# Performance work log

Hardware: AMD Instinct MI355X
Metric: run time of the kernel (lower is better)

## Reference

```python
import math
import jax, jax.numpy as jnp
import numpy as np

H = 1024
NH = 16
HD = H // NH
FF = 4096


def gelu_erf(x):
    return x * 0.5 * (1.0 + jax.lax.erf(x / jnp.sqrt(jnp.float32(2.0))))


def layernorm(x, gamma, beta, eps=1e-12):
    mean = x.mean(axis=-1, keepdims=True)
    var = ((x - mean) ** 2).mean(axis=-1, keepdims=True)
    return gamma * (x - mean) / jnp.sqrt(var + eps) + beta


def setup_inputs() -> dict:
    key = jax.random.key(0)
    ks = jax.random.split(key, 12)
    B, S = 2, 2048
    sc = 0.02
    return {
        "x": jax.random.normal(ks[0], (B, S, H), jnp.float32),
        "attention_mask": jnp.ones((B, S), jnp.int32),
        "Wq": jax.random.normal(ks[1], (H, H), jnp.float32) * sc,
        "bq": jnp.zeros((H,), jnp.float32),
        "Wk": jax.random.normal(ks[2], (H, H), jnp.float32) * sc,
        "bk": jnp.zeros((H,), jnp.float32),
        "Wv": jax.random.normal(ks[3], (H, H), jnp.float32) * sc,
        "bv": jnp.zeros((H,), jnp.float32),
        "Wo": jax.random.normal(ks[4], (H, H), jnp.float32) * sc,
        "bo": jnp.zeros((H,), jnp.float32),
        "ln1_g": jnp.ones((H,), jnp.float32),
        "ln1_b": jnp.zeros((H,), jnp.float32),
        "W1": jax.random.normal(ks[5], (H, FF), jnp.float32) * sc,
        "b1": jnp.zeros((FF,), jnp.float32),
        "W2": jax.random.normal(ks[6], (FF, H), jnp.float32) * sc,
        "b2": jnp.zeros((H,), jnp.float32),
        "ln2_g": jnp.ones((H,), jnp.float32),
        "ln2_b": jnp.zeros((H,), jnp.float32),
    }


def reference(x, attention_mask, Wq, bq, Wk, bk, Wv, bv, Wo, bo,
              ln1_g, ln1_b, W1, b1, W2, b2, ln2_g, ln2_b):
    B, S, _ = x.shape
    # QKV projections, split heads -> [B, NH, S, HD]
    def split(t):
        return t.reshape(B, S, NH, HD).transpose(0, 2, 1, 3)
    q = split(x @ Wq + bq)
    k = split(x @ Wk + bk)
    v = split(x @ Wv + bv)
    # scores [B, NH, S, S]
    s = jnp.einsum("bhqd,bhkd->bhqk", q, k) / math.sqrt(HD)
    mask = (attention_mask == 1)[:, None, None, :]  # [B,1,1,S]
    s = jnp.where(mask, s, -jnp.inf)
    p = jax.nn.softmax(s, axis=-1)
    a = jnp.einsum("bhqk,bhkd->bhqd", p, v)
    a = a.transpose(0, 2, 1, 3).reshape(B, S, H)  # merge heads
    a = a @ Wo + bo
    a = layernorm(a, ln1_g, ln1_b)  # NOTE: no residual in source
    m = gelu_erf(a @ W1 + b1) @ W2 + b2
    return layernorm(m, ln2_g, ln2_b)
```

## Files before the change

kernel.cpp:

```cpp
#include <hip/hip_runtime.h>
#include <hip/hip_bf16.h>
#include <math.h>

typedef __bf16 bf16;
typedef __attribute__((ext_vector_type(8))) __bf16 bf16x8;
typedef __attribute__((ext_vector_type(4))) __bf16 bf16x4;
typedef __attribute__((ext_vector_type(4))) float f32x4;

#define HDIM 1024
#define NHEAD 16
#define HD 64
#define FFDIM 4096
#define BATCH 2
#define SEQ 2048
#define M_TOK 4096
#define PSTRIDE ((size_t)M_TOK * HDIM)

static __device__ __forceinline__ void async_load16(const bf16* g, bf16* l) {
  __builtin_amdgcn_global_load_lds(
      (const __attribute__((address_space(1))) void*)g,
      (__attribute__((address_space(3))) void*)l, 16, 0, 0);
}

__global__ __launch_bounds__(256)
void cast_f32_to_bf16(const float* __restrict__ in, bf16* __restrict__ out)
{
  const size_t i = ((size_t)blockIdx.x * 256 + threadIdx.x) * 4;
  f32x4 v = *(const f32x4*)(in + i);
  bf16x4 o;
#pragma unroll
  for (int j = 0; j < 4; ++j) o[j] = (bf16)v[j];
  *(bf16x4*)(out + i) = o;
}

__global__ __launch_bounds__(256)
void transpose_cast(const float* __restrict__ in, bf16* __restrict__ out, int R, int C)
{
  __shared__ float tile[32][33];
  const int tx = threadIdx.x & 31, ty = threadIdx.x >> 5;
  const int c0 = blockIdx.x * 32, r0 = blockIdx.y * 32;
#pragma unroll
  for (int i = 0; i < 32; i += 8)
    tile[ty + i][tx] = in[(size_t)(r0 + ty + i) * C + c0 + tx];
  __syncthreads();
#pragma unroll
  for (int i = 0; i < 32; i += 8)
    out[(size_t)(c0 + ty + i) * R + r0 + tx] = (bf16)tile[tx][ty + i];
}

__global__ __launch_bounds__(256)
void transpose_cast4(const float* __restrict__ s0, const float* __restrict__ s1,
                     const float* __restrict__ s2, const float* __restrict__ s3,
                     bf16* __restrict__ dstBase)
{
  __shared__ float tile[32][33];
  const int z = blockIdx.z;
  const float* in = (z == 0) ? s0 : (z == 1) ? s1 : (z == 2) ? s2 : s3;
  bf16* out = dstBase + (size_t)z * HDIM * HDIM;
  const int tx = threadIdx.x & 31, ty = threadIdx.x >> 5;
  const int c0 = blockIdx.x * 32, r0 = blockIdx.y * 32;
#pragma unroll
  for (int i = 0; i < 32; i += 8)
    tile[ty + i][tx] = in[(size_t)(r0 + ty + i) * HDIM + c0 + tx];
  __syncthreads();
#pragma unroll
  for (int i = 0; i < 32; i += 8)
    out[(size_t)(c0 + ty + i) * HDIM + r0 + tx] = (bf16)tile[tx][ty + i];
}

template<int EPI>
__global__ __launch_bounds__(256)
void gemm_bt(const bf16* __restrict__ A, const bf16* __restrict__ Bt,
             const float* __restrict__ bias, void* __restrict__ Cout,
             int M, int N, int ldk, int kchunk)
{
  __shared__ __align__(16) bf16 As[128 * 64];
  __shared__ __align__(16) bf16 Bs[128 * 64];
  const int t = threadIdx.x;
  const int wave = t >> 6, lane = t & 63;
  const int lm = lane & 15, qd = lane >> 4;
  const int wm = (wave >> 1) * 64, wn = (wave & 1) * 64;
  const int bm = blockIdx.y * 128, bn = blockIdx.x * 128;
  const int kbeg = blockIdx.z * kchunk;

  f32x4 acc[4][4] = {};
  const int srow = t >> 3;
  const int schk = t & 7;

  for (int k0 = kbeg; k0 < kbeg + kchunk; k0 += 64) {
#pragma unroll
    for (int r = 0; r < 4; ++r) {
      const int row = r * 32 + srow;
      const int chunk = schk ^ (row & 7);
      async_load16(A + (size_t)(bm + row) * ldk + (k0 + chunk * 8),
                   (bf16*)((char*)As + r * 4096 + t * 16));
    }
#pragma unroll
    for (int r = 0; r < 4; ++r) {
      const int row = r * 32 + srow;
      const int chunk = schk ^ (row & 7);
      async_load16(Bt + (size_t)(bn + row) * ldk + (k0 + chunk * 8),
                   (bf16*)((char*)Bs + r * 4096 + t * 16));
    }
    __syncthreads();
#pragma unroll
    for (int ks = 0; ks < 2; ++ks) {
      bf16x8 av[4], bv[4];
#pragma unroll
      for (int mt = 0; mt < 4; ++mt) {
        const int row = wm + mt * 16 + lm;
        const int chunk = (ks * 4 + qd) ^ (row & 7);
        av[mt] = *(const bf16x8*)(As + row * 64 + chunk * 8);
      }
#pragma unroll
      for (int nt = 0; nt < 4; ++nt) {
        const int row = wn + nt * 16 + lm;
        const int chunk = (ks * 4 + qd) ^ (row & 7);
        bv[nt] = *(const bf16x8*)(Bs + row * 64 + chunk * 8);
      }
#pragma unroll
      for (int mt = 0; mt < 4; ++mt)
#pragma unroll
        for (int nt = 0; nt < 4; ++nt)
          acc[mt][nt] = __builtin_amdgcn_mfma_f32_16x16x32_bf16(av[mt], bv[nt], acc[mt][nt], 0, 0, 0);
    }
    __syncthreads();
  }

#pragma unroll
  for (int nt = 0; nt < 4; ++nt) {
    const int col = bn + wn + nt * 16 + lm;
    const float bs = (EPI == 1) ? 0.f : bias[col];
#pragma unroll
    for (int mt = 0; mt < 4; ++mt) {
#pragma unroll
      for (int r = 0; r < 4; ++r) {
        const int row = bm + wm + mt * 16 + qd * 4 + r;
        float v = acc[mt][nt][r] + bs;
        if (EPI == 1) {
          ((float*)Cout + (size_t)blockIdx.z * M * N)[(size_t)row * N + col] = v;
        } else if (EPI == 2) {
          float g = v * 0.5f * (1.0f + erff(v * 0.70710678118f));
          ((bf16*)Cout)[(size_t)row * N + col] = (bf16)g;
        } else {
          bf16* base = (bf16*)Cout;
          const int sect = col >> 10, c = col & 1023;
          if (sect < 2) {
            base[(size_t)sect * M_TOK * HDIM + (size_t)row * HDIM + c] = (bf16)v;
          } else {
            const int hh = c >> 6, dd = c & 63;
            const int bb = row >> 11, ss = row & 2047;
            base[(size_t)2 * M_TOK * HDIM +
                 (size_t)((bb * NHEAD + hh) * HD + dd) * SEQ + ss] = (bf16)v;
          }
        }
      }
    }
  }
}

__global__ __launch_bounds__(256)
void attn_kernel(const bf16* __restrict__ Q, const bf16* __restrict__ Kg,
                 const bf16* __restrict__ Vt, const int* __restrict__ mask,
                 bf16* __restrict__ Aout)
{
  __shared__ __align__(16) bf16 Ks[64 * 64];
  __shared__ __align__(16) bf16 Vs[64 * 64];
  __shared__ __align__(16) bf16 Ps[4][16 * 64];
  __shared__ float madd[64];

  const int t = threadIdx.x;
  const int wave = t >> 6, lane = t & 63;
  const int lm = lane & 15, qd = lane >> 4;
  const int bh = blockIdx.y;
  const int b = bh >> 4, h = bh & 15;
  const int q0 = blockIdx.x * 64;
  const int qg = q0 + wave * 16 + lm;
  bf16* Psw = Ps[wave];

  bf16x8 qf[2];
#pragma unroll
  for (int ks = 0; ks < 2; ++ks)
    qf[ks] = *(const bf16x8*)(Q + (size_t)(b * SEQ + qg) * HDIM + h * HD + ks * 32 + qd * 8);

  float l_lane = 0.f;
  f32x4 oacc[4] = {};

  const int srow = t >> 3, schk = t & 7;
  const float C = 0.1803368801f;

  for (int kv0 = 0; kv0 < SEQ; kv0 += 64) {
#pragma unroll
    for (int r = 0; r < 2; ++r) {
      const int row = r * 32 + srow;
      const int g = schk ^ (row & 7);
      async_load16(Kg + (size_t)(b * SEQ + kv0 + row) * HDIM + h * HD + g * 8,
                   (bf16*)((char*)Ks + r * 4096 + t * 16));
      async_load16(Vt + (size_t)(bh * HD + row) * SEQ + kv0 + g * 8,
                   (bf16*)((char*)Vs + r * 4096 + t * 16));
    }
    if (t < 64) madd[t] = (mask[b * SEQ + kv0 + t] == 1) ? 0.f : -1.0e30f;
    __syncthreads();

    f32x4 sacc[4] = {};
#pragma unroll
    for (int ks = 0; ks < 2; ++ks) {
#pragma unroll
      for (int nt = 0; nt < 4; ++nt) {
        const int row = nt * 16 + lm;
        const int c = (ks * 4 + qd) ^ (row & 7);
        bf16x8 kf = *(const bf16x8*)(Ks + row * 64 + c * 8);
        sacc[nt] = __builtin_amdgcn_mfma_f32_16x16x32_bf16(kf, qf[ks], sacc[nt], 0, 0, 0);
      }
    }

#pragma unroll
    for (int nt = 0; nt < 4; ++nt) {
      f32x4 ma = *(const f32x4*)(madd + nt * 16 + qd * 4);
      bf16x4 pk;
#pragma unroll
      for (int r = 0; r < 4; ++r) {
        const float pv = __builtin_amdgcn_exp2f(fmaf(sacc[nt][r], C, ma[r]));
        l_lane += pv;
        pk[r] = (bf16)pv;
      }
      *(bf16x4*)((char*)Psw + lm * 128 +
                 (((nt * 2 + (qd >> 1)) ^ (lm & 7)) * 16) + (qd & 1) * 8) = pk;
    }

#pragma unroll
    for (int ks = 0; ks < 2; ++ks) {
      bf16x8 pf = *(const bf16x8*)((char*)Psw + lm * 128 + (((ks * 4 + qd) ^ (lm & 7)) * 16));
#pragma unroll
      for (int nt = 0; nt < 4; ++nt) {
        const int row = nt * 16 + lm;
        const int c = (ks * 4 + qd) ^ (row & 7);
        bf16x8 vf = *(const bf16x8*)(Vs + row * 64 + c * 8);
        oacc[nt] = __builtin_amdgcn_mfma_f32_16x16x32_bf16(vf, pf, oacc[nt], 0, 0, 0);
      }
    }
    __syncthreads();
  }

  float l = l_lane;
  l += __shfl_xor(l, 16, 64);
  l += __shfl_xor(l, 32, 64);
  const float inv = 1.0f / l;

#pragma unroll
  for (int nt = 0; nt < 4; ++nt) {
    bf16x4 ok;
#pragma unroll
    for (int r = 0; r < 4; ++r) ok[r] = (bf16)(oacc[nt][r] * inv);
    *(bf16x4*)((char*)Psw + lm * 128 +
               (((nt * 2 + (qd >> 1)) ^ (lm & 7)) * 16) + (qd & 1) * 8) = ok;
  }
#pragma unroll
  for (int rr = 0; rr < 2; ++rr) {
    const int ql = rr * 8 + (lane >> 3);
    const int cl = lane & 7;
    bf16x8 v = *(const bf16x8*)((char*)Psw + ql * 128 + ((cl ^ (ql & 7)) * 16));
    *(bf16x8*)(Aout + (size_t)(b * SEQ + q0 + wave * 16 + ql) * HDIM + h * HD + cl * 8) = v;
  }
}

template<int NP, int OUT_BF16>
__global__ __launch_bounds__(256)
void ln_sum(const float* __restrict__ p, const float* __restrict__ bias,
            const float* __restrict__ gamma, const float* __restrict__ beta,
            void* __restrict__ out)
{
  const int row = blockIdx.x;
  const int t = threadIdx.x;
  f32x4 v = *(const f32x4*)(p + (size_t)row * HDIM + t * 4);
#pragma unroll
  for (int np = 1; np < NP; ++np) {
    f32x4 u = *(const f32x4*)(p + np * PSTRIDE + (size_t)row * HDIM + t * 4);
#pragma unroll
    for (int j = 0; j < 4; ++j) v[j] += u[j];
  }
  f32x4 bv0 = *(const f32x4*)(bias + t * 4);
#pragma unroll
  for (int j = 0; j < 4; ++j) v[j] += bv0[j];

  float s = v[0] + v[1] + v[2] + v[3];
  float s2 = v[0] * v[0] + v[1] * v[1] + v[2] * v[2] + v[3] * v[3];
#pragma unroll
  for (int d = 1; d < 64; d <<= 1) { s += __shfl_xor(s, d, 64); s2 += __shfl_xor(s2, d, 64); }
  __shared__ float ss[4], ss2[4];
  const int wave = t >> 6, lane = t & 63;
  if (lane == 0) { ss[wave] = s; ss2[wave] = s2; }
  __syncthreads();
  s = ss[0] + ss[1] + ss[2] + ss[3];
  s2 = ss2[0] + ss2[1] + ss2[2] + ss2[3];
  const float mean = s * (1.0f / HDIM);
  const float var = s2 * (1.0f / HDIM) - mean * mean;
  const float rstd = rsqrtf(var + 1e-12f);
  f32x4 gv = *(const f32x4*)(gamma + t * 4);
  f32x4 bv = *(const f32x4*)(beta + t * 4);
  f32x4 y;
#pragma unroll
  for (int j = 0; j < 4; ++j) y[j] = gv[j] * (v[j] - mean) * rstd + bv[j];
  if (OUT_BF16) {
    bf16x4 o;
#pragma unroll
    for (int j = 0; j < 4; ++j) o[j] = (bf16)y[j];
    *(bf16x4*)((bf16*)out + (size_t)row * HDIM + t * 4) = o;
  } else {
    *(f32x4*)((float*)out + (size_t)row * HDIM + t * 4) = y;
  }
}

extern "C" void kernel_launch(void* const* d_in, const int* in_sizes, int n_in,
                              void* d_out, int out_size, void* d_ws, size_t ws_size,
                              hipStream_t stream)
{
  const float* x    = (const float*)d_in[0];
  const int*   am   = (const int*)d_in[1];
  const float* Wq   = (const float*)d_in[2];
  const float* bq   = (const float*)d_in[3];
  const float* Wk   = (const float*)d_in[4];
  const float* bk   = (const float*)d_in[5];
  const float* Wv   = (const float*)d_in[6];
  const float* bv   = (const float*)d_in[7];
  const float* Wo   = (const float*)d_in[8];
  const float* bo   = (const float*)d_in[9];
  const float* ln1g = (const float*)d_in[10];
  const float* ln1b = (const float*)d_in[11];
  const float* W1   = (const float*)d_in[12];
  const float* b1   = (const float*)d_in[13];
  const float* W2   = (const float*)d_in[14];
  const float* b2   = (const float*)d_in[15];
  const float* ln2g = (const float*)d_in[16];
  const float* ln2b = (const float*)d_in[17];

  char* ws = (char*)d_ws;
  const size_t MB = 1ull << 20;
  bf16*  W1T  = (bf16*)(ws + 0 * MB);
  bf16*  W2T  = (bf16*)(ws + 8 * MB);
  bf16*  Xb   = (bf16*)(ws + 16 * MB);
  bf16*  QKVT = (bf16*)(ws + 24 * MB);
  bf16*  WoT  = (bf16*)(ws + 30 * MB);
  float* bqkv = (float*)(ws + 32 * MB);
  bf16*  Qb   = (bf16*)(ws + 33 * MB);
  bf16*  Kb   = (bf16*)(ws + 41 * MB);
  bf16*  Vtb  = (bf16*)(ws + 49 * MB);
  bf16*  Ab   = (bf16*)(ws + 16 * MB);
  float* Pw   = (float*)(ws + 33 * MB);
  bf16*  L1   = (bf16*)(ws + 65 * MB);
  bf16*  F1   = (bf16*)(ws + 16 * MB);
  float* Pf   = (float*)(ws + 48 * MB);

  cast_f32_to_bf16<<<M_TOK * HDIM / 1024, 256, 0, stream>>>(x, Xb);
  transpose_cast4<<<dim3(32, 32, 4), 256, 0, stream>>>(Wq, Wk, Wv, Wo, QKVT);
  transpose_cast<<<dim3(FFDIM / 32, HDIM / 32), 256, 0, stream>>>(W1, W1T, HDIM, FFDIM);
  transpose_cast<<<dim3(HDIM / 32, FFDIM / 32), 256, 0, stream>>>(W2, W2T, FFDIM, HDIM);
  hipMemcpyAsync(bqkv,        bq, HDIM * 4, hipMemcpyDeviceToDevice, stream);
  hipMemcpyAsync(bqkv + 1024, bk, HDIM * 4, hipMemcpyDeviceToDevice, stream);
  hipMemcpyAsync(bqkv + 2048, bv, HDIM * 4, hipMemcpyDeviceToDevice, stream);

  gemm_bt<3><<<dim3(3072 / 128, M_TOK / 128, 1), 256, 0, stream>>>(
      Xb, QKVT, bqkv, Qb, M_TOK, 3072, HDIM, HDIM);

  attn_kernel<<<dim3(SEQ / 64, BATCH * NHEAD), 256, 0, stream>>>(Qb, Kb, Vtb, am, Ab);

  gemm_bt<1><<<dim3(HDIM / 128, M_TOK / 128, 2), 256, 0, stream>>>(
      Ab, WoT, nullptr, Pw, M_TOK, HDIM, HDIM, 512);
  ln_sum<2, 1><<<M_TOK, 256, 0, stream>>>(Pw, bo, ln1g, ln1b, L1);

  gemm_bt<2><<<dim3(FFDIM / 128, M_TOK / 128, 1), 256, 0, stream>>>(
      L1, W1T, b1, F1, M_TOK, FFDIM, HDIM, HDIM);

  gemm_bt<1><<<dim3(HDIM / 128, M_TOK / 128, 2), 256, 0, stream>>>(
      F1, W2T, nullptr, Pf, M_TOK, HDIM, FFDIM, 2048);
  ln_sum<2, 0><<<M_TOK, 256, 0, stream>>>(Pf, b2, ln2g, ln2b, (float*)d_out);
}
```

Baseline: 395.2 us.

## Merge prep kernels, pass QKV biases directly, approximate erf, split-K 4 for W2

Merges the x cast and the four weight transpose/cast launches into one prep kernel, and drops the three bias memcpys by passing bq/bk/bv straight to the QKV GEMM epilogue. Replaces erff in the GELU epilogue with an Abramowitz-Stegun polynomial using hardware rcp and exp2, which lowers accuracy. When the workspace is large enough, the FFN down-projection uses split-K of 4 instead of 2, trading more fp32 partial traffic for more parallel blocks. These cut launch overhead and epilogue cost.

```diff
diff --git a/kernel.cpp b/kernel.cpp
--- a/kernel.cpp
+++ b/kernel.cpp
@@ -23,55 +23,58 @@
 }
 
 __global__ __launch_bounds__(256)
-void cast_f32_to_bf16(const float* __restrict__ in, bf16* __restrict__ out)
-{
-  const size_t i = ((size_t)blockIdx.x * 256 + threadIdx.x) * 4;
-  f32x4 v = *(const f32x4*)(in + i);
-  bf16x4 o;
-#pragma unroll
-  for (int j = 0; j < 4; ++j) o[j] = (bf16)v[j];
-  *(bf16x4*)(out + i) = o;
-}
-
-__global__ __launch_bounds__(256)
-void transpose_cast(const float* __restrict__ in, bf16* __restrict__ out, int R, int C)
-{
+void prep_kernel(const float* __restrict__ x,
+                 const float* __restrict__ Wq, const float* __restrict__ Wk,
+                 const float* __restrict__ Wv, const float* __restrict__ Wo,
+                 const float* __restrict__ W1, const float* __restrict__ W2,
+                 bf16* __restrict__ Xb, bf16* __restrict__ QKVT,
+                 bf16* __restrict__ W1T, bf16* __restrict__ W2T)
+{
+  const int z = blockIdx.z;
+  const int t = threadIdx.x;
+  if (z == 12) {
+    const size_t base = ((size_t)(blockIdx.y * 32 + blockIdx.x)) * 4096;
+#pragma unroll
+    for (int j = 0; j < 4; ++j) {
+      const size_t i = base + j * 1024 + t * 4;
+      f32x4 v = *(const f32x4*)(x + i);
+      bf16x4 o;
+#pragma unroll
+      for (int k = 0; k < 4; ++k) o[k] = (bf16)v[k];
+      *(bf16x4*)(Xb + i) = o;
+    }
+    return;
+  }
+  const float* ps; bf16* pd; int sld, dld;
+  if (z < 4) {
+    ps = (z == 0) ? Wq : (z == 1) ? Wk : (z == 2) ? Wv : Wo;
+    pd = QKVT + (size_t)z * HDIM * HDIM; sld = 1024; dld = 1024;
+  } else if (z < 8) {
+    const int c = z - 4;
+    ps = W1 + c * 1024; sld = 4096;
+    pd = W1T + (size_t)c * 1024 * 1024; dld = 1024;
+  } else {
+    const int c = z - 8;
+    ps = W2 + (size_t)c * 1024 * 1024; sld = 1024;
+    pd = W2T + c * 1024; dld = 4096;
+  }
   __shared__ float tile[32][33];
-  const int tx = threadIdx.x & 31, ty = threadIdx.x >> 5;
+  const int tx = t & 31, ty = t >> 5;
   const int c0 = blockIdx.x * 32, r0 = blockIdx.y * 32;
 #pragma unroll
   for (int i = 0; i < 32; i += 8)
-    tile[ty + i][tx] = in[(size_t)(r0 + ty + i) * C + c0 + tx];
+    tile[ty + i][tx] = ps[(size_t)(r0 + ty + i) * sld + c0 + tx];
   __syncthreads();
 #pragma unroll
   for (int i = 0; i < 32; i += 8)
-    out[(size_t)(c0 + ty + i) * R + r0 + tx] = (bf16)tile[tx][ty + i];
-}
-
-__global__ __launch_bounds__(256)
-void transpose_cast4(const float* __restrict__ s0, const float* __restrict__ s1,
-                     const float* __restrict__ s2, const float* __restrict__ s3,
-                     bf16* __restrict__ dstBase)
-{
-  __shared__ float tile[32][33];
-  const int z = blockIdx.z;
-  const float* in = (z == 0) ? s0 : (z == 1) ? s1 : (z == 2) ? s2 : s3;
-  bf16* out = dstBase + (size_t)z * HDIM * HDIM;
-  const int tx = threadIdx.x & 31, ty = threadIdx.x >> 5;
-  const int c0 = blockIdx.x * 32, r0 = blockIdx.y * 32;
-#pragma unroll
-  for (int i = 0; i < 32; i += 8)
-    tile[ty + i][tx] = in[(size_t)(r0 + ty + i) * HDIM + c0 + tx];
-  __syncthreads();
-#pragma unroll
-  for (int i = 0; i < 32; i += 8)
-    out[(size_t)(c0 + ty + i) * HDIM + r0 + tx] = (bf16)tile[tx][ty + i];
+    pd[(size_t)(c0 + ty + i) * dld + r0 + tx] = (bf16)tile[tx][ty + i];
 }
 
 template<int EPI>
 __global__ __launch_bounds__(256)
 void gemm_bt(const bf16* __restrict__ A, const bf16* __restrict__ Bt,
-             const float* __restrict__ bias, void* __restrict__ Cout,
+             const float* __restrict__ b0, const float* __restrict__ b1p,
+             const float* __restrict__ b2p, void* __restrict__ Cout,
              int M, int N, int ldk, int kchunk)
 {
   __shared__ __align__(16) bf16 As[128 * 64];
@@ -130,7 +133,12 @@
 #pragma unroll
   for (int nt = 0; nt < 4; ++nt) {
     const int col = bn + wn + nt * 16 + lm;
-    const float bs = (EPI == 1) ? 0.f : bias[col];
+    float bs = 0.f;
+    if (EPI == 2) bs = b0[col];
+    if (EPI == 3) {
+      const int sect = col >> 10, c = col & 1023;
+      bs = (sect == 0) ? b0[c] : (sect == 1) ? b1p[c] : b2p[c];
+    }
 #pragma unroll
     for (int mt = 0; mt < 4; ++mt) {
 #pragma unroll
@@ -140,7 +148,15 @@
         if (EPI == 1) {
           ((float*)Cout + (size_t)blockIdx.z * M * N)[(size_t)row * N + col] = v;
         } else if (EPI == 2) {
-          float g = v * 0.5f * (1.0f + erff(v * 0.70710678118f));
+          const float z = v * 0.70710678118f;
+          const float az = fabsf(z);
+          const float tt = __builtin_amdgcn_rcpf(fmaf(az, 0.3275911f, 1.0f));
+          const float poly = tt * fmaf(tt, fmaf(tt, fmaf(tt, fmaf(tt, 1.061405429f,
+                             -1.453152027f), 1.421413741f), -0.284496736f), 0.254829592f);
+          const float e = __builtin_amdgcn_exp2f(az * az * -1.4426950408889634f);
+          float erfv = 1.0f - poly * e;
+          erfv = (z < 0.f) ? -erfv : erfv;
+          const float g = 0.5f * v * (1.0f + erfv);
           ((bf16*)Cout)[(size_t)row * N + col] = (bf16)g;
         } else {
           bf16* base = (bf16*)Cout;
@@ -340,8 +356,7 @@
   bf16*  W2T  = (bf16*)(ws + 8 * MB);
   bf16*  Xb   = (bf16*)(ws + 16 * MB);
   bf16*  QKVT = (bf16*)(ws + 24 * MB);
-  bf16*  WoT  = (bf16*)(ws + 30 * MB);
-  float* bqkv = (float*)(ws + 32 * MB);
+  bf16*  WoT  = QKVT + (size_t)3 * HDIM * HDIM;
   bf16*  Qb   = (bf16*)(ws + 33 * MB);
   bf16*  Kb   = (bf16*)(ws + 41 * MB);
   bf16*  Vtb  = (bf16*)(ws + 49 * MB);
@@ -351,27 +366,28 @@
   bf16*  F1   = (bf16*)(ws + 16 * MB);
   float* Pf   = (float*)(ws + 48 * MB);
 
-  cast_f32_to_bf16<<<M_TOK * HDIM / 1024, 256, 0, stream>>>(x, Xb);
-  transpose_cast4<<<dim3(32, 32, 4), 256, 0, stream>>>(Wq, Wk, Wv, Wo, QKVT);
-  transpose_cast<<<dim3(FFDIM / 32, HDIM / 32), 256, 0, stream>>>(W1, W1T, HDIM, FFDIM);
-  transpose_cast<<<dim3(HDIM / 32, FFDIM / 32), 256, 0, stream>>>(W2, W2T, FFDIM, HDIM);
-  hipMemcpyAsync(bqkv,        bq, HDIM * 4, hipMemcpyDeviceToDevice, stream);
-  hipMemcpyAsync(bqkv + 1024, bk, HDIM * 4, hipMemcpyDeviceToDevice, stream);
-  hipMemcpyAsync(bqkv + 2048, bv, HDIM * 4, hipMemcpyDeviceToDevice, stream);
+  prep_kernel<<<dim3(32, 32, 13), 256, 0, stream>>>(x, Wq, Wk, Wv, Wo, W1, W2,
+                                                    Xb, QKVT, W1T, W2T);
 
   gemm_bt<3><<<dim3(3072 / 128, M_TOK / 128, 1), 256, 0, stream>>>(
-      Xb, QKVT, bqkv, Qb, M_TOK, 3072, HDIM, HDIM);
+      Xb, QKVT, bq, bk, bv, Qb, M_TOK, 3072, HDIM, HDIM);
 
   attn_kernel<<<dim3(SEQ / 64, BATCH * NHEAD), 256, 0, stream>>>(Qb, Kb, Vtb, am, Ab);
 
   gemm_bt<1><<<dim3(HDIM / 128, M_TOK / 128, 2), 256, 0, stream>>>(
-      Ab, WoT, nullptr, Pw, M_TOK, HDIM, HDIM, 512);
+      Ab, WoT, nullptr, nullptr, nullptr, Pw, M_TOK, HDIM, HDIM, 512);
   ln_sum<2, 1><<<M_TOK, 256, 0, stream>>>(Pw, bo, ln1g, ln1b, L1);
 
   gemm_bt<2><<<dim3(FFDIM / 128, M_TOK / 128, 1), 256, 0, stream>>>(
-      L1, W1T, b1, F1, M_TOK, FFDIM, HDIM, HDIM);
-
-  gemm_bt<1><<<dim3(HDIM / 128, M_TOK / 128, 2), 256, 0, stream>>>(
-      F1, W2T, nullptr, Pf, M_TOK, HDIM, FFDIM, 2048);
-  ln_sum<2, 0><<<M_TOK, 256, 0, stream>>>(Pf, b2, ln2g, ln2b, (float*)d_out);
-}
+      L1, W1T, b1, nullptr, nullptr, F1, M_TOK, FFDIM, HDIM, HDIM);
+
+  if (ws_size >= 113 * MB) {
+    gemm_bt<1><<<dim3(HDIM / 128, M_TOK / 128, 4), 256, 0, stream>>>(
+        F1, W2T, nullptr, nullptr, nullptr, Pf, M_TOK, HDIM, FFDIM, 1024);
+    ln_sum<4, 0><<<M_TOK, 256, 0, stream>>>(Pf, b2, ln2g, ln2b, (float*)d_out);
+  } else {
+    gemm_bt<1><<<dim3(HDIM / 128, M_TOK / 128, 2), 256, 0, stream>>>(
+        F1, W2T, nullptr, nullptr, nullptr, Pf, M_TOK, HDIM, FFDIM, 2048);
+    ln_sum<2, 0><<<M_TOK, 256, 0, stream>>>(Pf, b2, ln2g, ln2b, (float*)d_out);
+  }
+}
```

Result: faster. 385.3 us (-2.5%).
